# Kernel tuning notes

Hardware: AMD Instinct MI355X
Metric: run time of the kernel (lower is better)

Reference implementation:

```python
import jax, jax.numpy as jnp
import numpy as np
from jax import lax

DT = 0.1

def setup_inputs() -> dict:
    key = jax.random.key(0)
    ks = jax.random.split(key, 6)
    T, B, D, H, O = 4096, 16, 256, 256, 256
    x = jax.random.normal(ks[0], (T, B, D), dtype=jnp.float32)
    U_w = jax.random.normal(ks[1], (H, D), dtype=jnp.float32) / np.sqrt(D)
    U_b = jax.random.normal(ks[2], (H,), dtype=jnp.float32) * 0.1
    # underlying parameter of the ExpLambda parametrization: weight = expm(W_log)
    W_log = jax.random.normal(ks[3], (H, H), dtype=jnp.float32) * 0.01
    c_w = jax.random.normal(ks[4], (O, H), dtype=jnp.float32) / np.sqrt(H)
    c_b = jax.random.normal(ks[5], (O,), dtype=jnp.float32) * 0.1
    return {"x": x, "U_w": U_w, "U_b": U_b, "W_log": W_log, "c_w": c_w, "c_b": c_b}

def reference(x, U_w, U_b, W_log, c_w, c_b):
    # x: [T, B, D] (time-major, matching torch.transpose(x,0,1) in the original)
    T, B, D = x.shape
    H = W_log.shape[0]
    Wexp = jax.scipy.linalg.expm(W_log)          # parametrized recurrent weight
    u = jnp.einsum('tbd,hd->tbh', x, U_w) + U_b  # precompute U(x) for all steps

    def step(h, u_t):
        # h_next = h + dt * tanh(u_t - W h)
        h_next = h + DT * jnp.tanh(u_t - h @ Wexp.T)
        return h_next, h_next

    h0 = jnp.zeros((B, H), dtype=x.dtype)
    h_final, hidden = lax.scan(step, h0, u)       # hidden: [T, B, H]
    out = jnp.einsum('tbh,oh->tbo', hidden, c_w) + c_b
    # original returns h_next.unsqueeze(1) on a (1,B,H) tensor -> (1,1,B,H)
    return out, h_final[None, None]
```

## Files before the change

kernel.cpp:

```cpp
#include <hip/hip_runtime.h>
#include <math.h>

#define T_STEPS 4096
#define NB 16
#define NH 256
#define BH (NB * NH)
#define DT_STEP 0.1f

typedef __attribute__((ext_vector_type(8))) short short8;
typedef __attribute__((ext_vector_type(4))) float f32x4;

__global__ __launch_bounds__(1024) void k_init_S(const float* __restrict__ A,
                                                 float* __restrict__ S) {
    int idx = blockIdx.x * 1024 + threadIdx.x;
    int i = idx >> 8, j = idx & 255;
    S[idx] = A[idx] + (i == j ? 1.0f : 0.0f);
}

__global__ __launch_bounds__(256) void k_expm_term(const float* __restrict__ Pprev,
                                                   const float* __restrict__ A,
                                                   float* __restrict__ Pnew,
                                                   float* __restrict__ S,
                                                   float invk) {
    __shared__ float prow[256];
    int i = blockIdx.x, j = threadIdx.x;
    prow[j] = Pprev[i * 256 + j];
    __syncthreads();
    float acc = 0.f;
#pragma unroll 8
    for (int m = 0; m < 256; ++m) acc = fmaf(prow[m], A[m * 256 + j], acc);
    float v = acc * invk;
    Pnew[i * 256 + j] = v;
    S[i * 256 + j] += v;
}

__global__ __launch_bounds__(64) void k_pack_b(const float* __restrict__ W,
                                               unsigned int* __restrict__ P) {
    const int f = blockIdx.x;
    const int l = threadIdx.x;
    const int n  = ((f >> 3) << 4) | (l & 15);
    const int k0 = ((f & 7) << 5) | ((l >> 4) << 3);
    const float* sp = W + n * 256 + k0;
    unsigned int o0, o1, o2, o3;
    asm volatile("v_cvt_pk_bf16_f32 %0, %1, %2" : "=v"(o0) : "v"(sp[0]), "v"(sp[1]));
    asm volatile("v_cvt_pk_bf16_f32 %0, %1, %2" : "=v"(o1) : "v"(sp[2]), "v"(sp[3]));
    asm volatile("v_cvt_pk_bf16_f32 %0, %1, %2" : "=v"(o2) : "v"(sp[4]), "v"(sp[5]));
    asm volatile("v_cvt_pk_bf16_f32 %0, %1, %2" : "=v"(o3) : "v"(sp[6]), "v"(sp[7]));
    uint4* dst = (uint4*)(P + ((size_t)f * 64 + l) * 4);
    *dst = make_uint4(o0, o1, o2, o3);
}

__global__ __launch_bounds__(256) void k_gemm_mfma(const float* A,
                                                   const unsigned int* __restrict__ P,
                                                   const float* __restrict__ bias,
                                                   float* C) {
    const int tid = threadIdx.x;
    const int w = tid >> 6, l = tid & 63;
    const size_t r0 = (size_t)blockIdx.x * 64 + w * 16;
    const int arow = l & 15;
    const int kg   = l >> 4;

    union Frag { unsigned int u[4]; uint4 q; short8 v; };

    Frag af[8];
    const float* ap = A + (r0 + arow) * 256 + kg * 8;
#pragma unroll
    for (int kt = 0; kt < 8; ++kt) {
        float4 x0 = *(const float4*)(ap + kt * 32);
        float4 x1 = *(const float4*)(ap + kt * 32 + 4);
        asm volatile("v_cvt_pk_bf16_f32 %0, %1, %2" : "=v"(af[kt].u[0]) : "v"(x0.x), "v"(x0.y));
        asm volatile("v_cvt_pk_bf16_f32 %0, %1, %2" : "=v"(af[kt].u[1]) : "v"(x0.z), "v"(x0.w));
        asm volatile("v_cvt_pk_bf16_f32 %0, %1, %2" : "=v"(af[kt].u[2]) : "v"(x1.x), "v"(x1.y));
        asm volatile("v_cvt_pk_bf16_f32 %0, %1, %2" : "=v"(af[kt].u[3]) : "v"(x1.z), "v"(x1.w));
    }

    f32x4 acc[16];
#pragma unroll
    for (int nt = 0; nt < 16; ++nt) acc[nt] = f32x4{0.f, 0.f, 0.f, 0.f};

#pragma unroll
    for (int nt = 0; nt < 16; ++nt) {
#pragma unroll
        for (int kt = 0; kt < 8; ++kt) {
            Frag bf_;
            bf_.q = *(const uint4*)(P + (size_t)(((nt << 3) | kt) * 64 + l) * 4);
            acc[nt] = __builtin_amdgcn_mfma_f32_16x16x32_bf16(af[kt].v, bf_.v, acc[nt], 0, 0, 0);
        }
    }

#pragma unroll
    for (int nt = 0; nt < 16; ++nt) {
        float b = bias[(nt << 4) | arow];
        float* cp = C + (r0 + kg * 4) * 256 + (nt << 4) + arow;
#pragma unroll
        for (int r = 0; r < 4; ++r)
            cp[(size_t)r * 256] = acc[nt][r] + b;
    }
}

__global__ __launch_bounds__(512)
__attribute__((amdgpu_waves_per_eu(2, 2)))
void k_scan_bc6(const float* __restrict__ u,
                const float* S,
                float* hidden,
                float* __restrict__ hfin) {
    const int b   = blockIdx.x;
    const int tid = threadIdx.x;
    const int w   = tid >> 6;
    const int l   = tid & 63;
    const int lg  = l >> 4;
    const int lr  = l & 15;

    __shared__ unsigned int hlds[256];
    char* lds = (char*)hlds;

    union Frag { unsigned int u[4]; short8 v; };

    Frag ef[2][8];
#pragma unroll
    for (int j = 0; j < 2; ++j) {
        const int n = ((2 * w + j) << 4) | lr;
#pragma unroll
        for (int kt = 0; kt < 8; ++kt) {
            const int k0 = kt * 32 + lg * 8;
            const float* sp = S + (size_t)n * 256 + k0;
            float e[8];
#pragma unroll
            for (int q = 0; q < 8; ++q)
                e[q] = sp[q] - ((n == k0 + q) ? 1.0f : 0.0f);
#pragma unroll
            for (int r2 = 0; r2 < 4; ++r2) {
                unsigned int pk;
                asm volatile("v_cvt_pk_bf16_f32 %0, %1, %2"
                             : "=v"(pk) : "v"(e[2 * r2]), "v"(e[2 * r2 + 1]));
                ef[j][kt].u[r2] = pk;
            }
        }
    }

    const int j_own = (l >> 2) & 1;
    const int n_own = ((2 * w + j_own) << 4) | ((l >> 4) << 2) | (l & 3);
    const bool st = ((l & 8) == 0);
    const bool wrt = ((l & 9) == 0);

    if (tid < 256) hlds[tid] = 0u;

    const int NBLK = T_STEPS / 8;
    const size_t blkstride = 8 * (size_t)BH;

    float* hst = hidden + (size_t)b * NH + n_own;
    const float* uld = u + (size_t)b * NH + n_own + blkstride;

    float ucur[8], unxt[8], hsav[8];
    {
        const float* up0 = u + (size_t)b * NH + n_own;
#pragma unroll
        for (int q = 0; q < 8; ++q) ucur[q] = up0[q * (size_t)BH];
    }
    float hval = 0.f;
    __syncthreads();

    int roff = 0;
    for (int blk = 0; blk < NBLK; ++blk) {
#pragma unroll
        for (int s = 0; s < 8; ++s) {
            if (s == 0) {
                if (blk) {
#pragma unroll
                    for (int q = 0; q < 8; ++q)
                        if (st) hst[q * (size_t)BH] = hsav[q];
                }
#pragma unroll
                for (int q = 0; q < 8; ++q) unxt[q] = uld[q * (size_t)BH];
            }

            Frag hb[8];
#pragma unroll
            for (int kt = 0; kt < 8; ++kt)
                hb[kt].v = *(const short8*)(lds + roff + kt * 64 + lg * 16);

            f32x4 a0 = {0,0,0,0}, a1 = {0,0,0,0};
#pragma unroll
            for (int kt = 0; kt < 8; ++kt) {
                a0 = __builtin_amdgcn_mfma_f32_16x16x32_bf16(ef[0][kt].v, hb[kt].v, a0, 0, 0, 0);
                a1 = __builtin_amdgcn_mfma_f32_16x16x32_bf16(ef[1][kt].v, hb[kt].v, a1, 0, 0, 0);
            }

            f32x4 c = j_own ? a1 : a0;
            float y01 = (l & 1) ? c[1] : c[0];
            float y23 = (l & 1) ? c[3] : c[2];
            float y   = (l & 2) ? y23 : y01;

            float xa = (ucur[s] - hval) - y;
            float E2 = __expf(2.0f * xa);
            float th = fmaf(-2.0f, __builtin_amdgcn_rcpf(E2 + 1.0f), 1.0f);
            hval = fmaf(DT_STEP, th, hval);
            hsav[s] = hval;

            int nb = __builtin_amdgcn_mov_dpp(__float_as_int(hval), 0xB1, 0xF, 0xF, true);
            if (wrt) {
                unsigned int pk;
                asm volatile("v_cvt_pk_bf16_f32 %0, %1, %2"
                             : "=v"(pk) : "v"(hval), "v"(__int_as_float(nb)));
                *(unsigned int*)(lds + (roff ^ 512) + ((n_own >> 1) << 2)) = pk;
            }
            roff ^= 512;
            __syncthreads();
        }
#pragma unroll
        for (int q = 0; q < 8; ++q) ucur[q] = unxt[q];
        if (blk) hst += blkstride;
        if (blk <= NBLK - 3) uld += blkstride;
    }

#pragma unroll
    for (int q = 0; q < 8; ++q)
        if (st) hst[q * (size_t)BH] = hsav[q];
    if (st) hfin[(size_t)b * NH + n_own] = hval;
}

extern "C" void kernel_launch(void* const* d_in, const int* in_sizes, int n_in,
                              void* d_out, int out_size, void* d_ws, size_t ws_size,
                              hipStream_t stream) {
    const float* x     = (const float*)d_in[0];
    const float* U_w   = (const float*)d_in[1];
    const float* U_b   = (const float*)d_in[2];
    const float* W_log = (const float*)d_in[3];
    const float* c_w   = (const float*)d_in[4];
    const float* c_b   = (const float*)d_in[5];

    float* out    = (float*)d_out;
    float* hidden = out;
    float* hfin   = out + (long)T_STEPS * BH;

    float* ws = (float*)d_ws;
    float* S  = ws;
    float* Pa = ws + 65536;
    float* Pb = ws + 2 * 65536;
    float* u  = ws + 3 * 65536;

    k_init_S<<<64, 1024, 0, stream>>>(W_log, S);
    const float* prev = W_log;
    float* cur = Pa;
    for (int k = 2; k <= 9; ++k) {
        k_expm_term<<<256, 256, 0, stream>>>(prev, W_log, cur, S, 1.0f / (float)k);
        prev = cur;
        cur = (cur == Pa) ? Pb : Pa;
    }

    unsigned int* PUw = (unsigned int*)Pa;
    unsigned int* Pcw = (unsigned int*)Pb;
    k_pack_b<<<128, 64, 0, stream>>>(U_w, PUw);
    k_pack_b<<<128, 64, 0, stream>>>(c_w, Pcw);

    k_gemm_mfma<<<1024, 256, 0, stream>>>(x, PUw, U_b, u);

    k_scan_bc6<<<NB, 512, 0, stream>>>(u, S, hidden, hfin);

    k_gemm_mfma<<<1024, 256, 0, stream>>>(hidden, Pcw, c_b, hidden);
}
```

Before: 1.942 ms.

## Halve scan workgroup to 4 waves, each computing 64 hidden units

The recurrent scan kernel now runs 256 threads per batch row instead of 512, and each wave holds four 16-row weight tiles instead of two. The MFMA chain is split into independent accumulators across the K dimension, which shortens the dependent MFMA chain, and the partial sums are added at the end. Every lane now owns a unique hidden unit, so the redundant half-wave duplication and its store predicates go away. This cuts the per-step barrier cost by using fewer waves, but it doubles the MFMA work and register pressure per wave.

Measured after the change: 2.520 ms. +29.7%, slower.

```diff
diff --git a/kernel.cpp b/kernel.cpp
--- a/kernel.cpp
+++ b/kernel.cpp
@@ -98,9 +98,9 @@
     }
 }
 
-__global__ __launch_bounds__(512)
-__attribute__((amdgpu_waves_per_eu(2, 2)))
-void k_scan_bc6(const float* __restrict__ u,
+__global__ __launch_bounds__(256)
+__attribute__((amdgpu_waves_per_eu(1, 1)))
+void k_scan_bc7(const float* __restrict__ u,
                 const float* S,
                 float* hidden,
                 float* __restrict__ hfin) {
@@ -116,10 +116,10 @@
 
     union Frag { unsigned int u[4]; short8 v; };
 
-    Frag ef[2][8];
-#pragma unroll
-    for (int j = 0; j < 2; ++j) {
-        const int n = ((2 * w + j) << 4) | lr;
+    Frag ef[4][8];
+#pragma unroll
+    for (int j = 0; j < 4; ++j) {
+        const int n = ((4 * w + j) << 4) | lr;
 #pragma unroll
         for (int kt = 0; kt < 8; ++kt) {
             const int k0 = kt * 32 + lg * 8;
@@ -138,12 +138,11 @@
         }
     }
 
-    const int j_own = (l >> 2) & 1;
-    const int n_own = ((2 * w + j_own) << 4) | ((l >> 4) << 2) | (l & 3);
-    const bool st = ((l & 8) == 0);
-    const bool wrt = ((l & 9) == 0);
-
-    if (tid < 256) hlds[tid] = 0u;
+    const int j_own = (l >> 2) & 3;
+    const int n_own = (w << 6) | (j_own << 4) | (lg << 2) | (l & 3);
+    const bool wrt = ((l & 1) == 0);
+
+    hlds[tid] = 0u;
 
     const int NBLK = T_STEPS / 8;
     const size_t blkstride = 8 * (size_t)BH;
@@ -167,8 +166,7 @@
             if (s == 0) {
                 if (blk) {
 #pragma unroll
-                    for (int q = 0; q < 8; ++q)
-                        if (st) hst[q * (size_t)BH] = hsav[q];
+                    for (int q = 0; q < 8; ++q) hst[q * (size_t)BH] = hsav[q];
                 }
 #pragma unroll
                 for (int q = 0; q < 8; ++q) unxt[q] = uld[q * (size_t)BH];
@@ -179,16 +177,33 @@
             for (int kt = 0; kt < 8; ++kt)
                 hb[kt].v = *(const short8*)(lds + roff + kt * 64 + lg * 16);
 
-            f32x4 a0 = {0,0,0,0}, a1 = {0,0,0,0};
-#pragma unroll
-            for (int kt = 0; kt < 8; ++kt) {
-                a0 = __builtin_amdgcn_mfma_f32_16x16x32_bf16(ef[0][kt].v, hb[kt].v, a0, 0, 0, 0);
-                a1 = __builtin_amdgcn_mfma_f32_16x16x32_bf16(ef[1][kt].v, hb[kt].v, a1, 0, 0, 0);
-            }
-
-            f32x4 c = j_own ? a1 : a0;
-            float y01 = (l & 1) ? c[1] : c[0];
-            float y23 = (l & 1) ? c[3] : c[2];
+            f32x4 ac[4][4];
+#pragma unroll
+            for (int nt = 0; nt < 4; ++nt)
+#pragma unroll
+                for (int q = 0; q < 4; ++q) ac[nt][q] = f32x4{0.f, 0.f, 0.f, 0.f};
+#pragma unroll
+            for (int q = 0; q < 4; ++q)
+#pragma unroll
+                for (int nt = 0; nt < 4; ++nt)
+                    ac[nt][q] = __builtin_amdgcn_mfma_f32_16x16x32_bf16(
+                        ef[nt][q].v, hb[q].v, ac[nt][q], 0, 0, 0);
+#pragma unroll
+            for (int q = 0; q < 4; ++q)
+#pragma unroll
+                for (int nt = 0; nt < 4; ++nt)
+                    ac[nt][q] = __builtin_amdgcn_mfma_f32_16x16x32_bf16(
+                        ef[nt][q + 4].v, hb[q + 4].v, ac[nt][q], 0, 0, 0);
+
+            f32x4 s0 = (ac[0][0] + ac[0][1]) + (ac[0][2] + ac[0][3]);
+            f32x4 s1 = (ac[1][0] + ac[1][1]) + (ac[1][2] + ac[1][3]);
+            f32x4 s2 = (ac[2][0] + ac[2][1]) + (ac[2][2] + ac[2][3]);
+            f32x4 s3 = (ac[3][0] + ac[3][1]) + (ac[3][2] + ac[3][3]);
+            f32x4 ca = (j_own & 1) ? s1 : s0;
+            f32x4 cb = (j_own & 1) ? s3 : s2;
+            f32x4 cc = (j_own & 2) ? cb : ca;
+            float y01 = (l & 1) ? cc[1] : cc[0];
+            float y23 = (l & 1) ? cc[3] : cc[2];
             float y   = (l & 2) ? y23 : y01;
 
             float xa = (ucur[s] - hval) - y;
@@ -214,9 +229,8 @@
     }
 
 #pragma unroll
-    for (int q = 0; q < 8; ++q)
-        if (st) hst[q * (size_t)BH] = hsav[q];
-    if (st) hfin[(size_t)b * NH + n_own] = hval;
+    for (int q = 0; q < 8; ++q) hst[q * (size_t)BH] = hsav[q];
+    hfin[(size_t)b * NH + n_own] = hval;
 }
 
 extern "C" void kernel_launch(void* const* d_in, const int* in_sizes, int n_in,
@@ -255,7 +269,7 @@
 
     k_gemm_mfma<<<1024, 256, 0, stream>>>(x, PUw, U_b, u);
 
-    k_scan_bc6<<<NB, 512, 0, stream>>>(u, S, hidden, hfin);
+    k_scan_bc7<<<NB, 256, 0, stream>>>(u, S, hidden, hfin);
 
     k_gemm_mfma<<<1024, 256, 0, stream>>>(hidden, Pcw, c_b, hidden);
 }
```
